# Kernel tuning notes

Measured on AMD Instinct MI355X. Metric: run time of the kernel, lower is better.

## Reference

```python
import jax, jax.numpy as jnp
import numpy as np

MODEL_DIM = 512
NUM_HEADS = 8
HEAD_DIM = MODEL_DIM // NUM_HEADS  # 64
NUM_NODE = 1024
CLUSTER = 128
S = 60
EMBED = 0.5


def setup_inputs() -> dict:
    key = jax.random.key(0)
    ks = jax.random.split(key, 16)
    d = MODEL_DIM
    sc = 1.0 / np.sqrt(d)
    inp = {
        "x": jax.random.normal(ks[0], (4, 12, NUM_NODE, d), dtype=jnp.float32),
        "Wq": jax.random.normal(ks[1], (d, d), dtype=jnp.float32) * sc,
        "bq": jnp.zeros((d,), jnp.float32),
        "Wk": jax.random.normal(ks[2], (d, d), dtype=jnp.float32) * sc,
        "bk": jnp.zeros((d,), jnp.float32),
        "Wv": jax.random.normal(ks[3], (d, d), dtype=jnp.float32) * sc,
        "bv": jnp.zeros((d,), jnp.float32),
        "We": jax.random.normal(ks[4], (d, d), dtype=jnp.float32) * sc,
        "be": jnp.zeros((d,), jnp.float32),
        "Wo": jax.random.normal(ks[5], (d, d), dtype=jnp.float32) * sc,
        "bo": jnp.zeros((d,), jnp.float32),
        # adp_pos is initialized to zeros in torch; use small randn for a non-degenerate test
        "adp_pos": jax.random.normal(ks[6], (NUM_NODE, CLUSTER), dtype=jnp.float32) * 0.02,
        "U1": jax.random.normal(ks[7], (HEAD_DIM, S), dtype=jnp.float32) * np.sqrt(2.0 / (HEAD_DIM + S)),
        "U2": jax.random.normal(ks[8], (S, HEAD_DIM), dtype=jnp.float32) * np.sqrt(2.0 / (S + HEAD_DIM)),
    }
    return inp


def _split_heads(t):
    # torch.cat(torch.split(t, head_dim, -1), 0): heads stacked head-major on batch dim
    return jnp.concatenate(jnp.split(t, NUM_HEADS, axis=-1), axis=0)


def _merge_heads(t):
    return jnp.concatenate(jnp.split(t, NUM_HEADS, axis=0), axis=-1)


def _pool_nodes(t):
    # AdaptiveAvgPool2d((CLUSTER, None)) on (B,T,N,D) with N % CLUSTER == 0 -> block mean
    B, T, N, D = t.shape
    return t.reshape(B, T, CLUSTER, N // CLUSTER, D).mean(axis=3)


def reference(x, Wq, bq, Wk, bk, Wv, bv, We, be, Wo, bo, adp_pos, U1, U2):
    q = x @ Wq.T + bq                      # (B,T,N,D)
    k = _pool_nodes(x @ Wk.T + bk)          # (B,T,C,D)
    v = _pool_nodes(x @ Wv.T + bv)          # (B,T,C,D)
    ev = x @ We.T + be                      # (B,T,N,D)

    qh = _split_heads(q)                    # (B*H,T,N,d)
    kh = _split_heads(k)                    # (B*H,T,C,d)
    vh = _split_heads(v)                    # (B*H,T,C,d)
    evh = _split_heads(ev)                  # (B*H,T,N,d)

    # external attention branch: softmax over node dim (-2)
    exa = jax.nn.softmax(evh @ U1, axis=-2)  # (B*H,T,N,S)
    exa_val = (exa @ U2) * EMBED + evh       # (B*H,T,N,d)

    score = jnp.einsum("btnd,btcd->btnc", qh, kh) / np.sqrt(HEAD_DIM)
    score = score + adp_pos[None, None]      # (B*H,T,N,C)
    attn = jax.nn.softmax(score, axis=-1)

    out = attn @ vh + exa_val                # (B*H,T,N,d)
    out = _merge_heads(out)                  # (B,T,N,D)
    return out @ Wo.T + bo
```

## Files before the change

kernel.cpp:

```cpp
#include <hip/hip_runtime.h>


#define LOG2E 1.44269504088896f

typedef __attribute__((ext_vector_type(4))) float f32x4;
typedef __attribute__((ext_vector_type(8))) short bf16x8;

__device__ __forceinline__ unsigned short f2bf(float f) {
    union { float f; unsigned u; } v; v.f = f;
    unsigned r = (v.u + 0x7fffu + ((v.u >> 16) & 1u)) >> 16;
    return (unsigned short)r;
}
__device__ __forceinline__ float bf2f(unsigned short h) {
    union { unsigned u; float f; } v; v.u = ((unsigned)h) << 16;
    return v.f;
}

__global__ void cvt_w(const float* __restrict__ Wq, const float* __restrict__ Wk,
                      const float* __restrict__ Wv, const float* __restrict__ We,
                      const float* __restrict__ Wo, const float* __restrict__ U1,
                      const float* __restrict__ U2,
                      const float* __restrict__ bq, const float* __restrict__ bk,
                      const float* __restrict__ bv, const float* __restrict__ be,
                      unsigned short* __restrict__ Wqe, unsigned short* __restrict__ Wkv,
                      unsigned short* __restrict__ Wob, unsigned short* __restrict__ U1T,
                      unsigned short* __restrict__ U2bT,
                      float* __restrict__ bqe, float* __restrict__ bkv)
{
    int i = blockIdx.x * 256 + threadIdx.x;
    if (i < 524288) {
        int r = i >> 9;
        float v = (r < 512) ? Wq[i] : We[i - 262144];
        Wqe[i] = f2bf(v);
    } else if (i < 1048576) {
        int j = i - 524288; int r = j >> 9;
        float v = (r < 512) ? Wk[j] : Wv[j - 262144];
        Wkv[j] = f2bf(v);
    } else if (i < 1310720) {
        int j = i - 1048576;
        Wob[j] = f2bf(Wo[j]);
    } else if (i < 1314816) {
        int j = i - 1310720; int s = j >> 6, k = j & 63;
        U1T[j] = (s < 60) ? f2bf(U1[k * 60 + s]) : (unsigned short)0;
    } else if (i < 1318912) {
        int j = i - 1314816; int d = j >> 6, s = j & 63;
        U2bT[j] = (s < 60) ? f2bf(U2[s * 64 + d] * 0.5f) : (unsigned short)0;
    } else if (i < 1319936) {
        int j = i - 1318912;
        bqe[j] = (j < 512) ? bq[j] : be[j - 512];
    } else if (i < 1320960) {
        int j = i - 1319936;
        bkv[j] = (j < 512) ? bk[j] : bv[j - 512];
    }
}

__global__ void cvt_pool(const float* __restrict__ x, unsigned short* __restrict__ xb,
                         unsigned short* __restrict__ xpb)
{
    int i = blockIdx.x * 256 + threadIdx.x;
    int d4 = i & 127;
    int btc = i >> 7;
    int bt = btc >> 7, c = btc & 127;
    long base = ((long)(bt * 1024 + c * 8)) * 128 + d4;
    const float4* src = (const float4*)x + base;
    ushort4* dst = (ushort4*)xb + base;
    float sx = 0.f, sy = 0.f, sz = 0.f, sw = 0.f;
#pragma unroll
    for (int j = 0; j < 8; j++) {
        float4 v = src[(long)j * 128];
        sx += v.x; sy += v.y; sz += v.z; sw += v.w;
        ushort4 o;
        o.x = f2bf(v.x); o.y = f2bf(v.y); o.z = f2bf(v.z); o.w = f2bf(v.w);
        dst[(long)j * 128] = o;
    }
    ushort4 p;
    p.x = f2bf(sx * 0.125f); p.y = f2bf(sy * 0.125f);
    p.z = f2bf(sz * 0.125f); p.w = f2bf(sw * 0.125f);
    ((ushort4*)xpb)[(long)btc * 128 + d4] = p;
}

template <int OUTF32>
__global__ __launch_bounds__(256, 2) void gemm_bt(
    const unsigned short* __restrict__ A, const unsigned short* __restrict__ W,
    const float* __restrict__ bias, void* __restrict__ Cout,
    int M, int N, int K)
{
    __shared__ __attribute__((aligned(16))) unsigned short As[128 * 32];
    __shared__ __attribute__((aligned(16))) unsigned short Bs[128 * 32];
    const int tid = threadIdx.x;
    const int wave = tid >> 6, lane = tid & 63;
    const int quad = lane >> 4, l16 = lane & 15;
    const int m0 = blockIdx.x * 128, n0 = blockIdx.y * 128;
    const int wm = (wave & 1) * 64, wn = (wave >> 1) * 64;

    f32x4 acc[4][4];
#pragma unroll
    for (int i = 0; i < 4; i++)
#pragma unroll
        for (int j = 0; j < 4; j++) acc[i][j] = (f32x4){0.f, 0.f, 0.f, 0.f};

    const int c0 = tid, c1 = tid + 256;
    const int r0 = c0 >> 2, kc0 = (c0 & 3) * 8;
    const int r1 = c1 >> 2, kc1 = (c1 & 3) * 8;

    for (int k0 = 0; k0 < K; k0 += 32) {
        int4 a0 = *(const int4*)(A + (long)(m0 + r0) * K + k0 + kc0);
        int4 a1 = *(const int4*)(A + (long)(m0 + r1) * K + k0 + kc1);
        int4 b0 = *(const int4*)(W + (long)(n0 + r0) * K + k0 + kc0);
        int4 b1 = *(const int4*)(W + (long)(n0 + r1) * K + k0 + kc1);
        __syncthreads();
        *(int4*)&As[c0 * 8] = a0; *(int4*)&As[c1 * 8] = a1;
        *(int4*)&Bs[c0 * 8] = b0; *(int4*)&Bs[c1 * 8] = b1;
        __syncthreads();
        bf16x8 af[4], bfr[4];
#pragma unroll
        for (int t = 0; t < 4; t++)
            af[t] = *(const bf16x8*)&As[(wm + t * 16 + l16) * 32 + quad * 8];
#pragma unroll
        for (int t = 0; t < 4; t++)
            bfr[t] = *(const bf16x8*)&Bs[(wn + t * 16 + l16) * 32 + quad * 8];
#pragma unroll
        for (int tm = 0; tm < 4; tm++)
#pragma unroll
            for (int tn = 0; tn < 4; tn++)
                acc[tm][tn] = __builtin_amdgcn_mfma_f32_16x16x32_bf16(
                    af[tm], bfr[tn], acc[tm][tn], 0, 0, 0);
    }

#pragma unroll
    for (int tm = 0; tm < 4; tm++)
#pragma unroll
        for (int tn = 0; tn < 4; tn++) {
            int cc = n0 + wn + tn * 16 + l16;
            float bv = bias[cc];
#pragma unroll
            for (int r = 0; r < 4; r++) {
                int rr = m0 + wm + tm * 16 + quad * 4 + r;
                float v = acc[tm][tn][r] + bv;
                if (OUTF32) ((float*)Cout)[(long)rr * N + cc] = v;
                else        ((unsigned short*)Cout)[(long)rr * N + cc] = f2bf(v);
            }
        }
}

__global__ __launch_bounds__(256, 2) void g2_kv(
    const unsigned short* __restrict__ A, const unsigned short* __restrict__ W,
    const float* __restrict__ bias, unsigned short* __restrict__ kvK,
    unsigned short* __restrict__ vT)
{
    const int M = 6144, N = 1024, K = 512;
    __shared__ __attribute__((aligned(16))) unsigned short As[128 * 32];
    __shared__ __attribute__((aligned(16))) unsigned short Bs[128 * 32];
    const int tid = threadIdx.x;
    const int wave = tid >> 6, lane = tid & 63;
    const int quad = lane >> 4, l16 = lane & 15;
    const int m0 = blockIdx.x * 128, n0 = blockIdx.y * 128;
    const int wm = (wave & 1) * 64, wn = (wave >> 1) * 64;
    (void)M;

    f32x4 acc[4][4];
#pragma unroll
    for (int i = 0; i < 4; i++)
#pragma unroll
        for (int j = 0; j < 4; j++) acc[i][j] = (f32x4){0.f, 0.f, 0.f, 0.f};

    const int c0 = tid, c1 = tid + 256;
    const int r0 = c0 >> 2, kc0 = (c0 & 3) * 8;
    const int r1 = c1 >> 2, kc1 = (c1 & 3) * 8;

    for (int k0 = 0; k0 < K; k0 += 32) {
        int4 a0 = *(const int4*)(A + (long)(m0 + r0) * K + k0 + kc0);
        int4 a1 = *(const int4*)(A + (long)(m0 + r1) * K + k0 + kc1);
        int4 b0 = *(const int4*)(W + (long)(n0 + r0) * K + k0 + kc0);
        int4 b1 = *(const int4*)(W + (long)(n0 + r1) * K + k0 + kc1);
        __syncthreads();
        *(int4*)&As[c0 * 8] = a0; *(int4*)&As[c1 * 8] = a1;
        *(int4*)&Bs[c0 * 8] = b0; *(int4*)&Bs[c1 * 8] = b1;
        __syncthreads();
        bf16x8 af[4], bfr[4];
#pragma unroll
        for (int t = 0; t < 4; t++)
            af[t] = *(const bf16x8*)&As[(wm + t * 16 + l16) * 32 + quad * 8];
#pragma unroll
        for (int t = 0; t < 4; t++)
            bfr[t] = *(const bf16x8*)&Bs[(wn + t * 16 + l16) * 32 + quad * 8];
#pragma unroll
        for (int tm = 0; tm < 4; tm++)
#pragma unroll
            for (int tn = 0; tn < 4; tn++)
                acc[tm][tn] = __builtin_amdgcn_mfma_f32_16x16x32_bf16(
                    af[tm], bfr[tn], acc[tm][tn], 0, 0, 0);
    }

#pragma unroll
    for (int tm = 0; tm < 4; tm++)
#pragma unroll
        for (int tn = 0; tn < 4; tn++) {
            int cc = n0 + wn + tn * 16 + l16;
            float bv = bias[cc];
            int rrb = m0 + wm + tm * 16 + quad * 4;
            if (cc < 512) {
#pragma unroll
                for (int r = 0; r < 4; r++)
                    kvK[(long)(rrb + r) * 512 + cc] = f2bf(acc[tm][tn][r] + bv);
            } else {
                int hh = (cc - 512) >> 6, dd = (cc - 512) & 63;
                int btv = rrb >> 7, cv = rrb & 127;
                ushort4 o;
                o.x = f2bf(acc[tm][tn][0] + bv);
                o.y = f2bf(acc[tm][tn][1] + bv);
                o.z = f2bf(acc[tm][tn][2] + bv);
                o.w = f2bf(acc[tm][tn][3] + bv);
                *(ushort4*)(vT + ((long)(btv * 8 + hh) * 64 + dd) * 128 + cv) = o;
            }
        }
}

__global__ __launch_bounds__(256, 2) void ez_kernel(
    const unsigned short* __restrict__ qev, const unsigned short* __restrict__ U1T,
    unsigned short* __restrict__ Z)
{
    __shared__ __attribute__((aligned(16))) unsigned short evs[128 * 72];
    __shared__ __attribute__((aligned(16))) unsigned short u1s[64 * 72];
    int tid = threadIdx.x, bx = blockIdx.x;
    int bt = bx >> 6, h = (bx >> 3) & 7, nb = bx & 7;
    int wave = tid >> 6, lane = tid & 63, quad = lane >> 4, l16 = lane & 15;

#pragma unroll
    for (int i = 0; i < 4; i++) {
        int c = tid + i * 256; int row = c >> 3, kc = (c & 7) * 8;
        *(int4*)&evs[row * 72 + kc] =
            *(const int4*)(qev + ((long)(bt * 1024 + nb * 128 + row)) * 1024 + 512 + h * 64 + kc);
    }
#pragma unroll
    for (int i = 0; i < 2; i++) {
        int c = tid + i * 256; int row = c >> 3, kc = (c & 7) * 8;
        *(int4*)&u1s[row * 72 + kc] = *(const int4*)(U1T + row * 64 + kc);
    }
    __syncthreads();

    f32x4 acc[2][4];
#pragma unroll
    for (int i = 0; i < 2; i++)
#pragma unroll
        for (int t = 0; t < 4; t++) acc[i][t] = (f32x4){0.f, 0.f, 0.f, 0.f};

#pragma unroll
    for (int kt = 0; kt < 2; kt++) {
        bf16x8 a[2], b[4];
#pragma unroll
        for (int i = 0; i < 2; i++)
            a[i] = *(const bf16x8*)&evs[((wave * 2 + i) * 16 + l16) * 72 + kt * 32 + quad * 8];
#pragma unroll
        for (int t = 0; t < 4; t++)
            b[t] = *(const bf16x8*)&u1s[(t * 16 + l16) * 72 + kt * 32 + quad * 8];
#pragma unroll
        for (int i = 0; i < 2; i++)
#pragma unroll
            for (int t = 0; t < 4; t++)
                acc[i][t] = __builtin_amdgcn_mfma_f32_16x16x32_bf16(a[i], b[t], acc[i][t], 0, 0, 0);
    }

    long zb = (long)(bt * 8 + h) * 1024 + nb * 128;
#pragma unroll
    for (int i = 0; i < 2; i++)
#pragma unroll
        for (int t = 0; t < 4; t++) {
            int s = t * 16 + l16;
            if (s < 60) {
#pragma unroll
                for (int r = 0; r < 4; r++) {
                    int rr = (wave * 2 + i) * 16 + quad * 4 + r;
                    Z[(zb + rr) * 60 + s] = f2bf(acc[i][t][r]);
                }
            }
        }
}

__global__ __launch_bounds__(256, 2) void es_kernel(
    const unsigned short* __restrict__ Z, float* __restrict__ mS, float* __restrict__ lSinv)
{
    __shared__ float ms[4][64];
    __shared__ float ls[4][64];
    int tid = threadIdx.x;
    int s = tid & 63, g = tid >> 6;
    long zb = (long)blockIdx.x * 1024 * 60;
    float m = -1e30f, l = 0.f;
    if (s < 60) {
        for (int r = 0; r < 256; r++) {
            float z = bf2f(Z[zb + (long)(g * 256 + r) * 60 + s]);
            float nm = fmaxf(m, z);
            l = l * exp2f((m - nm) * LOG2E) + exp2f((z - nm) * LOG2E);
            m = nm;
        }
    }
    ms[g][s] = m; ls[g][s] = l;
    __syncthreads();
    if (tid < 60) {
        float M = fmaxf(fmaxf(ms[0][tid], ms[1][tid]), fmaxf(ms[2][tid], ms[3][tid]));
        float L = 0.f;
#pragma unroll
        for (int gg = 0; gg < 4; gg++) L += ls[gg][tid] * exp2f((ms[gg][tid] - M) * LOG2E);
        mS[blockIdx.x * 60 + tid] = M;
        lSinv[blockIdx.x * 60 + tid] = 1.0f / L;
    }
}

__global__ __launch_bounds__(256, 3) void att_kernel(
    const unsigned short* __restrict__ qev, const unsigned short* __restrict__ kvK,
    const unsigned short* __restrict__ vT, const unsigned short* __restrict__ Z,
    const float* __restrict__ mS, const float* __restrict__ lI,
    const float* __restrict__ adp, const unsigned short* __restrict__ U2bT,
    unsigned short* __restrict__ attn_out)
{
    __shared__ __attribute__((aligned(16))) unsigned short Ps[128 * 136];

    int tid = threadIdx.x, bx = blockIdx.x;
    int bt = bx >> 6, h = (bx >> 3) & 7, nb = bx & 7;
    int wave = tid >> 6, lane = tid & 63, quad = lane >> 4, l16 = lane & 15;
    int n0 = nb * 128;
    const int g = bt * 8 + h;
    const long qrow0 = (long)bt * 1024 + n0;

    f32x4 sc[2][8];
#pragma unroll
    for (int i = 0; i < 2; i++)
#pragma unroll
        for (int t = 0; t < 8; t++) sc[i][t] = (f32x4){0.f, 0.f, 0.f, 0.f};

#pragma unroll
    for (int kt = 0; kt < 2; kt++) {
        bf16x8 a[2];
#pragma unroll
        for (int i = 0; i < 2; i++)
            a[i] = *(const bf16x8*)(qev + (qrow0 + (wave * 2 + i) * 16 + l16) * 1024
                                    + h * 64 + kt * 32 + quad * 8);
#pragma unroll
        for (int tn = 0; tn < 8; tn++) {
            bf16x8 b = *(const bf16x8*)(kvK + (long)(bt * 128 + tn * 16 + l16) * 512
                                        + h * 64 + kt * 32 + quad * 8);
#pragma unroll
            for (int i = 0; i < 2; i++)
                sc[i][tn] = __builtin_amdgcn_mfma_f32_16x16x32_bf16(a[i], b, sc[i][tn], 0, 0, 0);
        }
    }

#pragma unroll
    for (int i = 0; i < 2; i++) {
#pragma unroll
        for (int tn = 0; tn < 8; tn++)
#pragma unroll
            for (int r = 0; r < 4; r++) {
                int rr = (wave * 2 + i) * 16 + quad * 4 + r;
                sc[i][tn][r] = sc[i][tn][r] * 0.125f + adp[(n0 + rr) * 128 + tn * 16 + l16];
            }
        float rmax[4], rsum[4];
#pragma unroll
        for (int r = 0; r < 4; r++) {
            float m = sc[i][0][r];
#pragma unroll
            for (int tn = 1; tn < 8; tn++) m = fmaxf(m, sc[i][tn][r]);
#pragma unroll
            for (int d = 1; d < 16; d <<= 1) m = fmaxf(m, __shfl_xor(m, d, 64));
            rmax[r] = m; rsum[r] = 0.f;
        }
#pragma unroll
        for (int tn = 0; tn < 8; tn++)
#pragma unroll
            for (int r = 0; r < 4; r++) {
                float p = exp2f((sc[i][tn][r] - rmax[r]) * LOG2E);
                sc[i][tn][r] = p; rsum[r] += p;
            }
#pragma unroll
        for (int r = 0; r < 4; r++) {
#pragma unroll
            for (int d = 1; d < 16; d <<= 1) rsum[r] += __shfl_xor(rsum[r], d, 64);
            rsum[r] = 1.0f / rsum[r];
        }
#pragma unroll
        for (int tn = 0; tn < 8; tn++)
#pragma unroll
            for (int r = 0; r < 4; r++) {
                int rr = (wave * 2 + i) * 16 + quad * 4 + r;
                Ps[rr * 136 + tn * 16 + l16] = f2bf(sc[i][tn][r] * rsum[r]);
            }
    }

    f32x4 oc[2][4];
#pragma unroll
    for (int i = 0; i < 2; i++)
#pragma unroll
        for (int t = 0; t < 4; t++) oc[i][t] = (f32x4){0.f, 0.f, 0.f, 0.f};

#pragma unroll
    for (int kt = 0; kt < 4; kt++) {
        bf16x8 a[2];
#pragma unroll
        for (int i = 0; i < 2; i++)
            a[i] = *(const bf16x8*)&Ps[((wave * 2 + i) * 16 + l16) * 136 + kt * 32 + quad * 8];
#pragma unroll
        for (int tn = 0; tn < 4; tn++) {
            bf16x8 b = *(const bf16x8*)(vT + ((long)g * 64 + tn * 16 + l16) * 128
                                        + kt * 32 + quad * 8);
#pragma unroll
            for (int i = 0; i < 2; i++)
                oc[i][tn] = __builtin_amdgcn_mfma_f32_16x16x32_bf16(a[i], b, oc[i][tn], 0, 0, 0);
        }
    }

#pragma unroll
    for (int kt = 0; kt < 2; kt++) {
        int sb = kt * 32 + quad * 8;
        float4 ma = *(const float4*)(mS + (long)g * 60 + sb);
        float4 mb2 = *(const float4*)(mS + (long)g * 60 + sb + 4);
        float4 la = *(const float4*)(lI + (long)g * 60 + sb);
        float4 lb2 = *(const float4*)(lI + (long)g * 60 + sb + 4);
        float mv[8] = {ma.x, ma.y, ma.z, ma.w, mb2.x, mb2.y, mb2.z, mb2.w};
        float lv[8] = {la.x, la.y, la.z, la.w, lb2.x, lb2.y, lb2.z, lb2.w};
        bf16x8 ea[2];
#pragma unroll
        for (int i = 0; i < 2; i++) {
            int row = (wave * 2 + i) * 16 + l16;
            const unsigned short* zp = Z + ((long)g * 1024 + n0 + row) * 60 + sb;
            uint2 z0 = *(const uint2*)zp;
            uint2 z1 = *(const uint2*)(zp + 4);
            unsigned zz[4] = {z0.x, z0.y, z1.x, z1.y};
            unsigned short es_[8];
#pragma unroll
            for (int j = 0; j < 8; j++) {
                unsigned short zh = (unsigned short)((zz[j >> 1] >> ((j & 1) * 16)) & 0xffff);
                float e = (sb + j < 60)
                    ? exp2f((bf2f(zh) - mv[j]) * LOG2E) * lv[j] : 0.f;
                es_[j] = f2bf(e);
            }
            ea[i] = *(bf16x8*)es_;
        }
#pragma unroll
        for (int tn = 0; tn < 4; tn++) {
            bf16x8 b = *(const bf16x8*)(U2bT + (tn * 16 + l16) * 64 + sb);
#pragma unroll
            for (int i = 0; i < 2; i++)
                oc[i][tn] = __builtin_amdgcn_mfma_f32_16x16x32_bf16(ea[i], b, oc[i][tn], 0, 0, 0);
        }
    }

#pragma unroll
    for (int i = 0; i < 2; i++)
#pragma unroll
        for (int tn = 0; tn < 4; tn++)
#pragma unroll
            for (int r = 0; r < 4; r++) {
                int rr = (wave * 2 + i) * 16 + quad * 4 + r;
                int cc = tn * 16 + l16;
                float ev = bf2f(qev[(qrow0 + rr) * 1024 + 512 + h * 64 + cc]);
                attn_out[(qrow0 + rr) * 512 + h * 64 + cc] = f2bf(oc[i][tn][r] + ev);
            }
}

extern "C" void kernel_launch(void* const* d_in, const int* in_sizes, int n_in,
                              void* d_out, int out_size, void* d_ws, size_t ws_size,
                              hipStream_t stream)
{
    const float* x   = (const float*)d_in[0];
    const float* Wq  = (const float*)d_in[1];
    const float* bq  = (const float*)d_in[2];
    const float* Wk  = (const float*)d_in[3];
    const float* bk  = (const float*)d_in[4];
    const float* Wv  = (const float*)d_in[5];
    const float* bv  = (const float*)d_in[6];
    const float* We  = (const float*)d_in[7];
    const float* be  = (const float*)d_in[8];
    const float* Wo  = (const float*)d_in[9];
    const float* bo  = (const float*)d_in[10];
    const float* adp = (const float*)d_in[11];
    const float* U1  = (const float*)d_in[12];
    const float* U2  = (const float*)d_in[13];

    char* ws = (char*)d_ws;
    unsigned short* xb   = (unsigned short*)(ws + 0);
    unsigned short* aout = xb;
    unsigned short* xpb  = (unsigned short*)(ws + 50331648);
    unsigned short* qev  = (unsigned short*)(ws + 56623104);
    unsigned short* kvK  = (unsigned short*)(ws + 157286400);
    unsigned short* vT   = (unsigned short*)(ws + 163577856);
    unsigned short* Zb   = (unsigned short*)(ws + 169869312);
    unsigned short* Wqe  = (unsigned short*)(ws + 217055232);
    unsigned short* Wkv  = (unsigned short*)(ws + 218103808);
    unsigned short* Wob  = (unsigned short*)(ws + 219152384);
    unsigned short* U1T  = (unsigned short*)(ws + 219676672);
    unsigned short* U2bT = (unsigned short*)(ws + 219684864);
    float*          mSb  = (float*)(ws + 219693056);
    float*          lIb  = (float*)(ws + 219785216);
    float*          bqe  = (float*)(ws + 219877376);
    float*          bkv  = (float*)(ws + 219881472);

    cvt_w<<<5160, 256, 0, stream>>>(Wq, Wk, Wv, We, Wo, U1, U2, bq, bk, bv, be,
                                    Wqe, Wkv, Wob, U1T, U2bT, bqe, bkv);
    cvt_pool<<<3072, 256, 0, stream>>>(x, xb, xpb);

    gemm_bt<0><<<dim3(384, 8), 256, 0, stream>>>(xb,  Wqe, bqe, (void*)qev, 49152, 1024, 512);
    g2_kv<<<dim3(48, 8), 256, 0, stream>>>(xpb, Wkv, bkv, kvK, vT);

    ez_kernel<<<3072, 256, 0, stream>>>(qev, U1T, Zb);
    es_kernel<<<384, 256, 0, stream>>>(Zb, mSb, lIb);
    att_kernel<<<3072, 256, 0, stream>>>(qev, kvK, vT, Zb, mSb, lIb, adp, U2bT, aout);

    gemm_bt<1><<<dim3(384, 4), 256, 0, stream>>>(aout, Wob, bo, d_out, 49152, 512, 512);
}
```

Measured before the change: 480.6 us.

## Use direct global-to-LDS loads in GEMMs, transpose score MFMA, widen es_kernel

The GEMM kernels now load tiles straight into LDS with global_load_lds instead of staging them through registers, and add a trailing barrier. Occupancy hints are raised. The 1/sqrt(d) scale is folded into Wq and bq. The attention score MFMA swaps its operands so each lane owns one query row, which allows vectorized adp loads, cheaper shuffle reductions and packed bf16 conversion. es_kernel uses 1024 threads per block so each thread scans fewer rows. The main risk is that the direct-LDS load layout must match the existing tile indexing, and the higher occupancy bounds may cause register spills.

```diff
diff --git a/kernel.cpp b/kernel.cpp
--- a/kernel.cpp
+++ b/kernel.cpp
@@ -14,6 +14,16 @@
 __device__ __forceinline__ float bf2f(unsigned short h) {
     union { unsigned u; float f; } v; v.u = ((unsigned)h) << 16;
     return v.f;
+}
+__device__ __forceinline__ unsigned cvt_pk_bf16(float lo, float hi) {
+    unsigned r;
+    asm("v_cvt_pk_bf16_f32 %0, %1, %2" : "=v"(r) : "v"(lo), "v"(hi));
+    return r;
+}
+__device__ __forceinline__ void gll16(const void* g, void* l) {
+    __builtin_amdgcn_global_load_lds((const __attribute__((address_space(1))) void*)g,
+                                     (__attribute__((address_space(3))) void*)l,
+                                     16, 0, 0);
 }
 
 __global__ void cvt_w(const float* __restrict__ Wq, const float* __restrict__ Wk,
@@ -30,7 +40,7 @@
     int i = blockIdx.x * 256 + threadIdx.x;
     if (i < 524288) {
         int r = i >> 9;
-        float v = (r < 512) ? Wq[i] : We[i - 262144];
+        float v = (r < 512) ? Wq[i] * 0.125f : We[i - 262144];
         Wqe[i] = f2bf(v);
     } else if (i < 1048576) {
         int j = i - 524288; int r = j >> 9;
@@ -47,7 +57,7 @@
         U2bT[j] = (s < 60) ? f2bf(U2[s * 64 + d] * 0.5f) : (unsigned short)0;
     } else if (i < 1319936) {
         int j = i - 1318912;
-        bqe[j] = (j < 512) ? bq[j] : be[j - 512];
+        bqe[j] = (j < 512) ? bq[j] * 0.125f : be[j - 512];
     } else if (i < 1320960) {
         int j = i - 1319936;
         bkv[j] = (j < 512) ? bk[j] : bv[j - 512];
@@ -80,7 +90,7 @@
 }
 
 template <int OUTF32>
-__global__ __launch_bounds__(256, 2) void gemm_bt(
+__global__ __launch_bounds__(256, 4) void gemm_bt(
     const unsigned short* __restrict__ A, const unsigned short* __restrict__ W,
     const float* __restrict__ bias, void* __restrict__ Cout,
     int M, int N, int K)
@@ -102,15 +112,20 @@
     const int c0 = tid, c1 = tid + 256;
     const int r0 = c0 >> 2, kc0 = (c0 & 3) * 8;
     const int r1 = c1 >> 2, kc1 = (c1 & 3) * 8;
+    const unsigned short* pa0 = A + (long)(m0 + r0) * K + kc0;
+    const unsigned short* pa1 = A + (long)(m0 + r1) * K + kc1;
+    const unsigned short* pb0 = W + (long)(n0 + r0) * K + kc0;
+    const unsigned short* pb1 = W + (long)(n0 + r1) * K + kc1;
+    unsigned short* lA0 = &As[wave * 512];
+    unsigned short* lA1 = &As[2048 + wave * 512];
+    unsigned short* lB0 = &Bs[wave * 512];
+    unsigned short* lB1 = &Bs[2048 + wave * 512];
 
     for (int k0 = 0; k0 < K; k0 += 32) {
-        int4 a0 = *(const int4*)(A + (long)(m0 + r0) * K + k0 + kc0);
-        int4 a1 = *(const int4*)(A + (long)(m0 + r1) * K + k0 + kc1);
-        int4 b0 = *(const int4*)(W + (long)(n0 + r0) * K + k0 + kc0);
-        int4 b1 = *(const int4*)(W + (long)(n0 + r1) * K + k0 + kc1);
-        __syncthreads();
-        *(int4*)&As[c0 * 8] = a0; *(int4*)&As[c1 * 8] = a1;
-        *(int4*)&Bs[c0 * 8] = b0; *(int4*)&Bs[c1 * 8] = b1;
+        gll16(pa0 + k0, lA0);
+        gll16(pa1 + k0, lA1);
+        gll16(pb0 + k0, lB0);
+        gll16(pb1 + k0, lB1);
         __syncthreads();
         bf16x8 af[4], bfr[4];
 #pragma unroll
@@ -125,6 +140,7 @@
             for (int tn = 0; tn < 4; tn++)
                 acc[tm][tn] = __builtin_amdgcn_mfma_f32_16x16x32_bf16(
                     af[tm], bfr[tn], acc[tm][tn], 0, 0, 0);
+        __syncthreads();
     }
 
 #pragma unroll
@@ -143,12 +159,12 @@
         }
 }
 
-__global__ __launch_bounds__(256, 2) void g2_kv(
+__global__ __launch_bounds__(256, 4) void g2_kv(
     const unsigned short* __restrict__ A, const unsigned short* __restrict__ W,
     const float* __restrict__ bias, unsigned short* __restrict__ kvK,
     unsigned short* __restrict__ vT)
 {
-    const int M = 6144, N = 1024, K = 512;
+    const int K = 512;
     __shared__ __attribute__((aligned(16))) unsigned short As[128 * 32];
     __shared__ __attribute__((aligned(16))) unsigned short Bs[128 * 32];
     const int tid = threadIdx.x;
@@ -156,7 +172,6 @@
     const int quad = lane >> 4, l16 = lane & 15;
     const int m0 = blockIdx.x * 128, n0 = blockIdx.y * 128;
     const int wm = (wave & 1) * 64, wn = (wave >> 1) * 64;
-    (void)M;
 
     f32x4 acc[4][4];
 #pragma unroll
@@ -167,15 +182,20 @@
     const int c0 = tid, c1 = tid + 256;
     const int r0 = c0 >> 2, kc0 = (c0 & 3) * 8;
     const int r1 = c1 >> 2, kc1 = (c1 & 3) * 8;
+    const unsigned short* pa0 = A + (long)(m0 + r0) * K + kc0;
+    const unsigned short* pa1 = A + (long)(m0 + r1) * K + kc1;
+    const unsigned short* pb0 = W + (long)(n0 + r0) * K + kc0;
+    const unsigned short* pb1 = W + (long)(n0 + r1) * K + kc1;
+    unsigned short* lA0 = &As[wave * 512];
+    unsigned short* lA1 = &As[2048 + wave * 512];
+    unsigned short* lB0 = &Bs[wave * 512];
+    unsigned short* lB1 = &Bs[2048 + wave * 512];
 
     for (int k0 = 0; k0 < K; k0 += 32) {
-        int4 a0 = *(const int4*)(A + (long)(m0 + r0) * K + k0 + kc0);
-        int4 a1 = *(const int4*)(A + (long)(m0 + r1) * K + k0 + kc1);
-        int4 b0 = *(const int4*)(W + (long)(n0 + r0) * K + k0 + kc0);
-        int4 b1 = *(const int4*)(W + (long)(n0 + r1) * K + k0 + kc1);
-        __syncthreads();
-        *(int4*)&As[c0 * 8] = a0; *(int4*)&As[c1 * 8] = a1;
-        *(int4*)&Bs[c0 * 8] = b0; *(int4*)&Bs[c1 * 8] = b1;
+        gll16(pa0 + k0, lA0);
+        gll16(pa1 + k0, lA1);
+        gll16(pb0 + k0, lB0);
+        gll16(pb1 + k0, lB1);
         __syncthreads();
         bf16x8 af[4], bfr[4];
 #pragma unroll
@@ -190,6 +210,7 @@
             for (int tn = 0; tn < 4; tn++)
                 acc[tm][tn] = __builtin_amdgcn_mfma_f32_16x16x32_bf16(
                     af[tm], bfr[tn], acc[tm][tn], 0, 0, 0);
+        __syncthreads();
     }
 
 #pragma unroll
@@ -277,18 +298,18 @@
         }
 }
 
-__global__ __launch_bounds__(256, 2) void es_kernel(
+__global__ __launch_bounds__(1024, 4) void es_kernel(
     const unsigned short* __restrict__ Z, float* __restrict__ mS, float* __restrict__ lSinv)
 {
-    __shared__ float ms[4][64];
-    __shared__ float ls[4][64];
+    __shared__ float ms[16][64];
+    __shared__ float ls[16][64];
     int tid = threadIdx.x;
     int s = tid & 63, g = tid >> 6;
     long zb = (long)blockIdx.x * 1024 * 60;
     float m = -1e30f, l = 0.f;
     if (s < 60) {
-        for (int r = 0; r < 256; r++) {
-            float z = bf2f(Z[zb + (long)(g * 256 + r) * 60 + s]);
+        for (int r = 0; r < 64; r++) {
+            float z = bf2f(Z[zb + (long)(g * 64 + r) * 60 + s]);
             float nm = fmaxf(m, z);
             l = l * exp2f((m - nm) * LOG2E) + exp2f((z - nm) * LOG2E);
             m = nm;
@@ -297,16 +318,18 @@
     ms[g][s] = m; ls[g][s] = l;
     __syncthreads();
     if (tid < 60) {
-        float M = fmaxf(fmaxf(ms[0][tid], ms[1][tid]), fmaxf(ms[2][tid], ms[3][tid]));
+        float M = ms[0][tid];
+#pragma unroll
+        for (int gg = 1; gg < 16; gg++) M = fmaxf(M, ms[gg][tid]);
         float L = 0.f;
 #pragma unroll
-        for (int gg = 0; gg < 4; gg++) L += ls[gg][tid] * exp2f((ms[gg][tid] - M) * LOG2E);
+        for (int gg = 0; gg < 16; gg++) L += ls[gg][tid] * exp2f((ms[gg][tid] - M) * LOG2E);
         mS[blockIdx.x * 60 + tid] = M;
         lSinv[blockIdx.x * 60 + tid] = 1.0f / L;
     }
 }
 
-__global__ __launch_bounds__(256, 3) void att_kernel(
+__global__ __launch_bounds__(256, 4) void att_kernel(
     const unsigned short* __restrict__ qev, const unsigned short* __restrict__ kvK,
     const unsigned short* __restrict__ vT, const unsigned short* __restrict__ Z,
     const float* __restrict__ mS, const float* __restrict__ lI,
@@ -330,60 +353,53 @@
 
 #pragma unroll
     for (int kt = 0; kt < 2; kt++) {
-        bf16x8 a[2];
+        bf16x8 qf[2];
 #pragma unroll
         for (int i = 0; i < 2; i++)
-            a[i] = *(const bf16x8*)(qev + (qrow0 + (wave * 2 + i) * 16 + l16) * 1024
-                                    + h * 64 + kt * 32 + quad * 8);
+            qf[i] = *(const bf16x8*)(qev + (qrow0 + wave * 32 + i * 16 + l16) * 1024
+                                     + h * 64 + kt * 32 + quad * 8);
 #pragma unroll
         for (int tn = 0; tn < 8; tn++) {
-            bf16x8 b = *(const bf16x8*)(kvK + (long)(bt * 128 + tn * 16 + l16) * 512
-                                        + h * 64 + kt * 32 + quad * 8);
+            bf16x8 kf = *(const bf16x8*)(kvK + (long)(bt * 128 + tn * 16 + l16) * 512
+                                         + h * 64 + kt * 32 + quad * 8);
 #pragma unroll
             for (int i = 0; i < 2; i++)
-                sc[i][tn] = __builtin_amdgcn_mfma_f32_16x16x32_bf16(a[i], b, sc[i][tn], 0, 0, 0);
+                sc[i][tn] = __builtin_amdgcn_mfma_f32_16x16x32_bf16(kf, qf[i], sc[i][tn], 0, 0, 0);
         }
     }
 
 #pragma unroll
     for (int i = 0; i < 2; i++) {
+        const int qr = wave * 32 + i * 16 + l16;
+        float m = -1e30f;
+#pragma unroll
+        for (int tn = 0; tn < 8; tn++) {
+            float4 ad = *(const float4*)(adp + (long)(n0 + qr) * 128 + tn * 16 + quad * 4);
+            sc[i][tn][0] += ad.x; sc[i][tn][1] += ad.y;
+            sc[i][tn][2] += ad.z; sc[i][tn][3] += ad.w;
+#pragma unroll
+            for (int r = 0; r < 4; r++) m = fmaxf(m, sc[i][tn][r]);
+        }
+        m = fmaxf(m, __shfl_xor(m, 16, 64));
+        m = fmaxf(m, __shfl_xor(m, 32, 64));
+        float s = 0.f;
 #pragma unroll
         for (int tn = 0; tn < 8; tn++)
 #pragma unroll
             for (int r = 0; r < 4; r++) {
-                int rr = (wave * 2 + i) * 16 + quad * 4 + r;
-                sc[i][tn][r] = sc[i][tn][r] * 0.125f + adp[(n0 + rr) * 128 + tn * 16 + l16];
+                float p = exp2f((sc[i][tn][r] - m) * LOG2E);
+                sc[i][tn][r] = p; s += p;
             }
-        float rmax[4], rsum[4];
-#pragma unroll
-        for (int r = 0; r < 4; r++) {
-            float m = sc[i][0][r];
-#pragma unroll
-            for (int tn = 1; tn < 8; tn++) m = fmaxf(m, sc[i][tn][r]);
-#pragma unroll
-            for (int d = 1; d < 16; d <<= 1) m = fmaxf(m, __shfl_xor(m, d, 64));
-            rmax[r] = m; rsum[r] = 0.f;
-        }
-#pragma unroll
-        for (int tn = 0; tn < 8; tn++)
-#pragma unroll
-            for (int r = 0; r < 4; r++) {
-                float p = exp2f((sc[i][tn][r] - rmax[r]) * LOG2E);
-                sc[i][tn][r] = p; rsum[r] += p;
-            }
-#pragma unroll
-        for (int r = 0; r < 4; r++) {
-#pragma unroll
-            for (int d = 1; d < 16; d <<= 1) rsum[r] += __shfl_xor(rsum[r], d, 64);
-            rsum[r] = 1.0f / rsum[r];
-        }
-#pragma unroll
-        for (int tn = 0; tn < 8; tn++)
-#pragma unroll
-            for (int r = 0; r < 4; r++) {
-                int rr = (wave * 2 + i) * 16 + quad * 4 + r;
-                Ps[rr * 136 + tn * 16 + l16] = f2bf(sc[i][tn][r] * rsum[r]);
-            }
+        s += __shfl_xor(s, 16, 64);
+        s += __shfl_xor(s, 32, 64);
+        float rinv = 1.0f / s;
+#pragma unroll
+        for (int tn = 0; tn < 8; tn++) {
+            uint2 w2;
+            w2.x = cvt_pk_bf16(sc[i][tn][0] * rinv, sc[i][tn][1] * rinv);
+            w2.y = cvt_pk_bf16(sc[i][tn][2] * rinv, sc[i][tn][3] * rinv);
+            *(uint2*)&Ps[qr * 136 + tn * 16 + quad * 4] = w2;
+        }
     }
 
     f32x4 oc[2][4];
@@ -502,7 +518,7 @@
     g2_kv<<<dim3(48, 8), 256, 0, stream>>>(xpb, Wkv, bkv, kvK, vT);
 
     ez_kernel<<<3072, 256, 0, stream>>>(qev, U1T, Zb);
-    es_kernel<<<384, 256, 0, stream>>>(Zb, mSb, lIb);
+    es_kernel<<<384, 1024, 0, stream>>>(Zb, mSb, lIb);
     att_kernel<<<3072, 256, 0, stream>>>(qev, kvK, vT, Zb, mSb, lIb, adp, U2bT, aout);
 
     gemm_bt<1><<<dim3(384, 4), 256, 0, stream>>>(aout, Wob, bo, d_out, 49152, 512, 512);
```

Result: no change. 473.9 us (-1.4%).
